# Performance work log

Measured on AMD Instinct MI355X. Metric: run time of the kernel, lower is better.

## Reference

```python
import jax, jax.numpy as jnp
import numpy as np

N = 50000
E = 800000
D_IN = 128
D_EMB = 128
D_OUT = 2
AGGRS = ('sum', 'max', 'mean', 'sum', 'max', 'mean')


def setup_inputs() -> dict:
    key = jax.random.key(0)
    ks = jax.random.split(key, 10)
    x = jax.random.normal(ks[0], (N, D_IN), dtype=jnp.float32)
    edge_index = jax.random.randint(ks[1], (2, E), 0, N, dtype=jnp.int64)
    # 6 SAGEConv layers, all 128->128: lin_l (weight+bias, applied to aggregated
    # neighbors) and lin_r (weight only, applied to root/self features).
    w_l = jax.random.normal(ks[2], (6, D_EMB, D_EMB), dtype=jnp.float32) * 0.05
    b_l = jax.random.normal(ks[3], (6, D_EMB), dtype=jnp.float32) * 0.05
    w_r = jax.random.normal(ks[4], (6, D_EMB, D_EMB), dtype=jnp.float32) * 0.05
    w1 = jax.random.normal(ks[5], (D_EMB, D_EMB), dtype=jnp.float32) * 0.05
    b1 = jax.random.normal(ks[6], (D_EMB,), dtype=jnp.float32) * 0.05
    w2 = jax.random.normal(ks[7], (D_EMB, D_OUT), dtype=jnp.float32) * 0.05
    b2 = jax.random.normal(ks[8], (D_OUT,), dtype=jnp.float32) * 0.05
    return {"x": x, "edge_index": edge_index, "w_l": w_l, "b_l": b_l,
            "w_r": w_r, "w1": w1, "b1": b1, "w2": w2, "b2": b2}


def _aggregate(msg, dst, aggr, num_nodes):
    # msg: [E, D] gathered source features; dst: [E] target node ids.
    if aggr == 'sum':
        return jax.ops.segment_sum(msg, dst, num_segments=num_nodes)
    if aggr == 'max':
        m = jax.ops.segment_max(msg, dst, num_segments=num_nodes)
        # nodes with no incoming edges -> 0 (PyG scatter-max fill)
        return jnp.where(jnp.isfinite(m), m, 0.0)
    # mean
    s = jax.ops.segment_sum(msg, dst, num_segments=num_nodes)
    cnt = jax.ops.segment_sum(jnp.ones((msg.shape[0],), msg.dtype), dst,
                              num_segments=num_nodes)
    return s / jnp.maximum(cnt, 1.0)[:, None]


def _sage_conv(x, src, dst, wl, bl, wr, aggr):
    msg = x[src]                               # [E, D] gather
    agg = _aggregate(msg, dst, aggr, x.shape[0])
    return agg @ wl + bl + x @ wr              # lin_l(aggr) + lin_r(x)


def reference(x, edge_index, w_l, b_l, w_r, w1, b1, w2, b2):
    src, dst = edge_index[0], edge_index[1]    # messages flow src -> dst
    h = x
    for i, aggr in enumerate(AGGRS):
        h = _sage_conv(h, src, dst, w_l[i], b_l[i], w_r[i], aggr)
        h = jax.nn.relu(h)                     # dropout p=0.1 is identity in eval
    h = jax.nn.relu(h @ w1 + b1)
    return h @ w2 + b2
```

## Files before the change

kernel.cpp:

```cpp
#include <hip/hip_runtime.h>

#define NN 50000
#define NE 800000
#define D 128

typedef unsigned short ushort_t;
typedef __attribute__((ext_vector_type(8))) short short8;
typedef __attribute__((ext_vector_type(4))) float f32x4;
typedef __attribute__((ext_vector_type(8))) _Float16 half8;
typedef __attribute__((ext_vector_type(2))) _Float16 half2v;


__global__ void k_hist(const int* __restrict__ dst, int* __restrict__ cnt, int e) {
  int i = blockIdx.x * blockDim.x + threadIdx.x;
  if (i < e) atomicAdd(&cnt[dst[i]], 1);
}

__global__ __launch_bounds__(1024) void k_scan(const int* __restrict__ cnt,
                                               int* __restrict__ row_start,
                                               int* __restrict__ cursor, int n) {
  __shared__ int wsum[16];
  __shared__ int carry_s;
  int t = threadIdx.x;
  int lane = t & 63, wid = t >> 6;
  if (t == 0) carry_s = 0;
  __syncthreads();
  for (int base = 0; base < n; base += 4096) {
    int i = base + t * 4;
    int4 v = make_int4(0, 0, 0, 0);
    if (i + 3 < n) v = *(const int4*)&cnt[i];
    else if (i < n) {
      v.x = cnt[i];
      if (i + 1 < n) v.y = cnt[i + 1];
      if (i + 2 < n) v.z = cnt[i + 2];
    }
    int tot = v.x + v.y + v.z + v.w;
    int x = tot;
    #pragma unroll
    for (int off = 1; off < 64; off <<= 1) {
      int y = __shfl_up(x, off, 64);
      if (lane >= off) x += y;
    }
    if (lane == 63) wsum[wid] = x;
    __syncthreads();
    if (wid == 0) {
      int w = (lane < 16) ? wsum[lane] : 0;
      #pragma unroll
      for (int off = 1; off < 16; off <<= 1) {
        int y = __shfl_up(w, off, 64);
        if (lane >= off) w += y;
      }
      if (lane < 16) wsum[lane] = w;
    }
    __syncthreads();
    int off0 = carry_s + (wid ? wsum[wid - 1] : 0) + (x - tot);
    int4 o;
    o.x = off0;
    o.y = off0 + v.x;
    o.z = off0 + v.x + v.y;
    o.w = off0 + v.x + v.y + v.z;
    if (i + 3 < n) {
      *(int4*)&row_start[i] = o;
      *(int4*)&cursor[i] = o;
    } else if (i < n) {
      row_start[i] = o.x; cursor[i] = o.x;
      if (i + 1 < n) { row_start[i + 1] = o.y; cursor[i + 1] = o.y; }
      if (i + 2 < n) { row_start[i + 2] = o.z; cursor[i + 2] = o.z; }
    }
    __syncthreads();
    if (t == 0) carry_s += wsum[15];
    __syncthreads();
  }
  if (t == 0) row_start[n] = carry_s;
}

__global__ __launch_bounds__(256) void k_scatter(const int* __restrict__ src,
                                                 const int* __restrict__ dst,
                                                 int* __restrict__ cursor,
                                                 int* __restrict__ csr_src, int e) {
  int g = blockIdx.x & 7;
  int i = (blockIdx.x >> 3) * 1024 + threadIdx.x * 4;
  if (i >= e) return;
  int4 s4 = *(const int4*)&src[i];
  int4 d4 = *(const int4*)&dst[i];
  if ((unsigned)d4.x / 6250u == (unsigned)g) { int p = atomicAdd(&cursor[d4.x], 1); csr_src[p] = s4.x; }
  if ((unsigned)d4.y / 6250u == (unsigned)g) { int p = atomicAdd(&cursor[d4.y], 1); csr_src[p] = s4.y; }
  if ((unsigned)d4.z / 6250u == (unsigned)g) { int p = atomicAdd(&cursor[d4.z], 1); csr_src[p] = s4.z; }
  if ((unsigned)d4.w / 6250u == (unsigned)g) { int p = atomicAdd(&cursor[d4.w], 1); csr_src[p] = s4.w; }
}


__global__ __launch_bounds__(256) void k_tofp16(const float* __restrict__ in,
                                                _Float16* __restrict__ out, int n8) {
  int i = blockIdx.x * 256 + threadIdx.x;
  if (i >= n8) return;
  float4 a = ((const float4*)in)[i * 2];
  float4 b = ((const float4*)in)[i * 2 + 1];
  half8 o;
  o[0] = (_Float16)a.x; o[1] = (_Float16)a.y; o[2] = (_Float16)a.z; o[3] = (_Float16)a.w;
  o[4] = (_Float16)b.x; o[5] = (_Float16)b.y; o[6] = (_Float16)b.z; o[7] = (_Float16)b.w;
  ((half8*)out)[i] = o;
}


__global__ void k_wsplit(const float* __restrict__ W, ushort_t* __restrict__ hi,
                         ushort_t* __restrict__ lo, int total) {
  int idx = blockIdx.x * 256 + threadIdx.x;
  if (idx >= total) return;
  int mat = idx >> 14, rem = idx & 16383;
  int k = rem >> 7, c = rem & 127;
  float f = W[idx];
  unsigned u = __float_as_uint(f);
  float lf = f - __uint_as_float(u & 0xffff0000u);
  size_t dst = ((size_t)mat << 14) + (size_t)(k >> 5) * 4096 + c * 32 + (k & 31);
  hi[dst] = (ushort_t)(u >> 16);
  lo[dst] = (ushort_t)(__float_as_uint(lf) >> 16);
}


__device__ __forceinline__ float4 op_add(float4 a, float4 v) {
  a.x += v.x; a.y += v.y; a.z += v.z; a.w += v.w; return a;
}
__device__ __forceinline__ float4 op_max(float4 a, float4 v) {
  a.x = fmaxf(a.x, v.x); a.y = fmaxf(a.y, v.y);
  a.z = fmaxf(a.z, v.z); a.w = fmaxf(a.w, v.w); return a;
}
__device__ __forceinline__ void h8_to_f(half8 v, float4& x, float4& y) {
  x.x = (float)v[0]; x.y = (float)v[1]; x.z = (float)v[2]; x.w = (float)v[3];
  y.x = (float)v[4]; y.y = (float)v[5]; y.z = (float)v[6]; y.w = (float)v[7];
}

template <int AGGR>
__global__ __launch_bounds__(256) void k_aggregate(const _Float16* __restrict__ h,
                                                   const int* __restrict__ csr_src,
                                                   const int* __restrict__ row_start,
                                                   _Float16* __restrict__ agg, int n) {
  int lane = threadIdx.x & 63;
  int node = blockIdx.x * 4 + (threadIdx.x >> 6);
  if (node >= n) return;
  int slot = lane >> 4, c = lane & 15;
  const half8* __restrict__ hp = (const half8*)h;
  int s = row_start[node], e = row_start[node + 1];
  float4 init;
  if (AGGR == 1) init = make_float4(-INFINITY, -INFINITY, -INFINITY, -INFINITY);
  else           init = make_float4(0.f, 0.f, 0.f, 0.f);
  float4 a0x = init, a0y = init, a1x = init, a1y = init;
  int j = s + slot;
  for (; j + 4 < e; j += 8) {
    int i0 = csr_src[j], i1 = csr_src[j + 4];
    half8 v0 = hp[(size_t)i0 * 16 + c];
    half8 v1 = hp[(size_t)i1 * 16 + c];
    float4 v0x, v0y, v1x, v1y;
    h8_to_f(v0, v0x, v0y);
    h8_to_f(v1, v1x, v1y);
    if (AGGR == 1) {
      a0x = op_max(a0x, v0x); a0y = op_max(a0y, v0y);
      a1x = op_max(a1x, v1x); a1y = op_max(a1y, v1y);
    } else {
      a0x = op_add(a0x, v0x); a0y = op_add(a0y, v0y);
      a1x = op_add(a1x, v1x); a1y = op_add(a1y, v1y);
    }
  }
  for (; j < e; j += 4) {
    half8 v0 = hp[(size_t)csr_src[j] * 16 + c];
    float4 v0x, v0y;
    h8_to_f(v0, v0x, v0y);
    if (AGGR == 1) { a0x = op_max(a0x, v0x); a0y = op_max(a0y, v0y); }
    else           { a0x = op_add(a0x, v0x); a0y = op_add(a0y, v0y); }
  }
  float4 rx, ry;
  if (AGGR == 1) { rx = op_max(a0x, a1x); ry = op_max(a0y, a1y); }
  else           { rx = op_add(a0x, a1x); ry = op_add(a0y, a1y); }
  #pragma unroll
  for (int off = 16; off <= 32; off <<= 1) {
    float4 ox, oy;
    ox.x = __shfl_xor(rx.x, off, 64); ox.y = __shfl_xor(rx.y, off, 64);
    ox.z = __shfl_xor(rx.z, off, 64); ox.w = __shfl_xor(rx.w, off, 64);
    oy.x = __shfl_xor(ry.x, off, 64); oy.y = __shfl_xor(ry.y, off, 64);
    oy.z = __shfl_xor(ry.z, off, 64); oy.w = __shfl_xor(ry.w, off, 64);
    if (AGGR == 1) { rx = op_max(rx, ox); ry = op_max(ry, oy); }
    else           { rx = op_add(rx, ox); ry = op_add(ry, oy); }
  }
  if (slot == 0) {
    if (AGGR == 1) {
      if (e == s) { rx = make_float4(0.f,0.f,0.f,0.f); ry = rx; }
    } else if (AGGR == 2) {
      float inv = 1.0f / fmaxf((float)(e - s), 1.0f);
      rx.x *= inv; rx.y *= inv; rx.z *= inv; rx.w *= inv;
      ry.x *= inv; ry.y *= inv; ry.z *= inv; ry.w *= inv;
    }
    half8 o;
    o[0] = (_Float16)rx.x; o[1] = (_Float16)rx.y; o[2] = (_Float16)rx.z; o[3] = (_Float16)rx.w;
    o[4] = (_Float16)ry.x; o[5] = (_Float16)ry.y; o[6] = (_Float16)ry.z; o[7] = (_Float16)ry.w;
    ((half8*)agg)[(size_t)node * 16 + c] = o;
  }
}


#define GBM 64

__global__ __launch_bounds__(256) void k_gemm(
    const _Float16* __restrict__ A1, const ushort_t* __restrict__ Wh1, const ushort_t* __restrict__ Wl1,
    const _Float16* __restrict__ A2, const ushort_t* __restrict__ Wh2, const ushort_t* __restrict__ Wl2,
    const float* __restrict__ bias, _Float16* __restrict__ out, int M, int has2) {
  __shared__ ushort_t Ah[GBM * 40];
  __shared__ ushort_t Al[GBM * 40];
  __shared__ ushort_t Bh[128 * 40];
  __shared__ ushort_t Bl[128 * 40];
  int t = threadIdx.x;
  int lane = t & 63, wid = t >> 6;
  int wr = wid >> 1, wc = wid & 1;
  int l15 = lane & 15, kg = lane >> 4;
  int row0 = blockIdx.x * GBM;

  f32x4 acc[2][4] = {};

  int nmat = has2 ? 2 : 1;
  for (int mat = 0; mat < nmat; ++mat) {
    const _Float16* __restrict__ A = mat ? A2 : A1;
    const ushort_t* __restrict__ Wh = mat ? Wh2 : Wh1;
    const ushort_t* __restrict__ Wl = mat ? Wl2 : Wl1;
    for (int kt = 0; kt < 4; ++kt) {
      __syncthreads();
      {
        int r = t >> 2, cq = t & 3;
        int grow = row0 + r;
        half8 v = {};
        if (grow < M) v = *(const half8*)&A[(size_t)grow * D + kt * 32 + cq * 8];
        unsigned hw[8], lw[8];
        #pragma unroll
        for (int eidx = 0; eidx < 8; ++eidx) {
          float f = (float)v[eidx];
          unsigned u = __float_as_uint(f);
          float lf = f - __uint_as_float(u & 0xffff0000u);
          hw[eidx] = u >> 16;
          lw[eidx] = __float_as_uint(lf) >> 16;
        }
        uint4 hv = make_uint4(hw[0] | (hw[1] << 16), hw[2] | (hw[3] << 16),
                              hw[4] | (hw[5] << 16), hw[6] | (hw[7] << 16));
        uint4 lv = make_uint4(lw[0] | (lw[1] << 16), lw[2] | (lw[3] << 16),
                              lw[4] | (lw[5] << 16), lw[6] | (lw[7] << 16));
        *(uint4*)&Ah[r * 40 + cq * 8] = hv;
        *(uint4*)&Al[r * 40 + cq * 8] = lv;
      }
      {
        int c = t >> 1, q = t & 1;
        const ushort_t* sh = Wh + (size_t)kt * 4096 + t * 16;
        const ushort_t* sl = Wl + (size_t)kt * 4096 + t * 16;
        uint4 a0 = *(const uint4*)sh;
        uint4 a1 = *(const uint4*)(sh + 8);
        uint4 b0 = *(const uint4*)sl;
        uint4 b1 = *(const uint4*)(sl + 8);
        *(uint4*)&Bh[c * 40 + q * 16]     = a0;
        *(uint4*)&Bh[c * 40 + q * 16 + 8] = a1;
        *(uint4*)&Bl[c * 40 + q * 16]     = b0;
        *(uint4*)&Bl[c * 40 + q * 16 + 8] = b1;
      }
      __syncthreads();
      short8 ah[2], al[2], bh[4], bl[4];
      #pragma unroll
      for (int m = 0; m < 2; ++m) {
        int row = wr * 32 + m * 16 + l15;
        ah[m] = *(const short8*)&Ah[row * 40 + kg * 8];
        al[m] = *(const short8*)&Al[row * 40 + kg * 8];
      }
      #pragma unroll
      for (int n = 0; n < 4; ++n) {
        int col = wc * 64 + n * 16 + l15;
        bh[n] = *(const short8*)&Bh[col * 40 + kg * 8];
        bl[n] = *(const short8*)&Bl[col * 40 + kg * 8];
      }
      #pragma unroll
      for (int m = 0; m < 2; ++m)
        #pragma unroll
        for (int n = 0; n < 4; ++n) {
          acc[m][n] = __builtin_amdgcn_mfma_f32_16x16x32_bf16(ah[m], bh[n], acc[m][n], 0, 0, 0);
          acc[m][n] = __builtin_amdgcn_mfma_f32_16x16x32_bf16(ah[m], bl[n], acc[m][n], 0, 0, 0);
          acc[m][n] = __builtin_amdgcn_mfma_f32_16x16x32_bf16(al[m], bh[n], acc[m][n], 0, 0, 0);
        }
    }
  }
  int crow = kg * 4;
  #pragma unroll
  for (int n = 0; n < 4; ++n) {
    int col = wc * 64 + n * 16 + l15;
    float b = bias[col];
    #pragma unroll
    for (int m = 0; m < 2; ++m) {
      int rbase = row0 + wr * 32 + m * 16 + crow;
      #pragma unroll
      for (int q = 0; q < 4; ++q) {
        int grow = rbase + q;
        if (grow < M)
          out[(size_t)grow * D + col] = (_Float16)fmaxf(acc[m][n][q] + b, 0.f);
      }
    }
  }
}


__global__ __launch_bounds__(256) void k_head(const _Float16* __restrict__ h,
                                              const float* __restrict__ w2,
                                              const float* __restrict__ b2,
                                              float* __restrict__ out, int n) {
  int lane = threadIdx.x & 63;
  int node = blockIdx.x * 4 + (threadIdx.x >> 6);
  if (node >= n) return;
  half2v v = *(const half2v*)&h[(size_t)node * D + lane * 2];
  float v0 = (float)v[0], v1 = (float)v[1];
  float4 w = *(const float4*)&w2[lane * 4];
  float p0 = v0 * w.x + v1 * w.z;
  float p1 = v0 * w.y + v1 * w.w;
  #pragma unroll
  for (int off = 32; off; off >>= 1) {
    p0 += __shfl_xor(p0, off, 64);
    p1 += __shfl_xor(p1, off, 64);
  }
  if (lane == 0)
    ((float2*)out)[node] = make_float2(p0 + b2[0], p1 + b2[1]);
}


extern "C" void kernel_launch(void* const* d_in, const int* in_sizes, int n_in,
                              void* d_out, int out_size, void* d_ws, size_t ws_size,
                              hipStream_t stream) {
  const float* x   = (const float*)d_in[0];
  const int*   ei  = (const int*)d_in[1];
  const float* w_l = (const float*)d_in[2];
  const float* b_l = (const float*)d_in[3];
  const float* w_r = (const float*)d_in[4];
  const float* w1  = (const float*)d_in[5];
  const float* b1  = (const float*)d_in[6];
  const float* w2  = (const float*)d_in[7];
  const float* b2  = (const float*)d_in[8];
  float* out = (float*)d_out;

  const int* src = ei;
  const int* dst = ei + NE;

  char* ws = (char*)d_ws;
  size_t SZH = (size_t)NN * D * sizeof(_Float16);
  _Float16* bufX = (_Float16*)ws;
  _Float16* bufA = (_Float16*)(ws + SZH);
  _Float16* bufB = (_Float16*)(ws + 2 * SZH);
  int* csr_src   = (int*)(ws + 3 * SZH);
  int* row_start = (int*)(ws + 3 * SZH + (size_t)NE * sizeof(int));
  int* cursor    = row_start + NN + 2;
  int* cnt       = cursor + NN + 2;
  ushort_t* whi  = (ushort_t*)(cnt + NN + 2);
  ushort_t* wlo  = whi + 13 * 16384;

  k_wsplit<<<(6 * 16384 + 255) / 256, 256, 0, stream>>>(w_l, whi, wlo, 6 * 16384);
  k_wsplit<<<(6 * 16384 + 255) / 256, 256, 0, stream>>>(w_r, whi + 6 * 16384, wlo + 6 * 16384, 6 * 16384);
  k_wsplit<<<(16384 + 255) / 256, 256, 0, stream>>>(w1, whi + 12 * 16384, wlo + 12 * 16384, 16384);
  k_tofp16<<<(NN * D / 8 + 255) / 256, 256, 0, stream>>>(x, bufX, NN * D / 8);

  hipMemsetAsync(cnt, 0, NN * sizeof(int), stream);
  k_hist<<<(NE + 255) / 256, 256, 0, stream>>>(dst, cnt, NE);
  k_scan<<<1, 1024, 0, stream>>>(cnt, row_start, cursor, NN);
  k_scatter<<<8 * ((NE + 1023) / 1024), 256, 0, stream>>>(src, dst, cursor, csr_src, NE);

  const int agg_grid  = (NN + 3) / 4;
  const int gemm_grid = (NN + GBM - 1) / GBM;

  const _Float16* h = bufX;
  _Float16* bufs[2] = {bufA, bufB};
  for (int i = 0; i < 6; ++i) {
    _Float16* aggb = bufs[i & 1];
    switch (i % 3) {
      case 0: k_aggregate<0><<<agg_grid, 256, 0, stream>>>(h, csr_src, row_start, aggb, NN); break;
      case 1: k_aggregate<1><<<agg_grid, 256, 0, stream>>>(h, csr_src, row_start, aggb, NN); break;
      case 2: k_aggregate<2><<<agg_grid, 256, 0, stream>>>(h, csr_src, row_start, aggb, NN); break;
    }
    k_gemm<<<gemm_grid, 256, 0, stream>>>(aggb, whi + (size_t)i * 16384, wlo + (size_t)i * 16384,
                                          h,    whi + (size_t)(6 + i) * 16384, wlo + (size_t)(6 + i) * 16384,
                                          b_l + (size_t)i * D, aggb, NN, 1);
    h = aggb;
  }
  k_gemm<<<gemm_grid, 256, 0, stream>>>(h, whi + (size_t)12 * 16384, wlo + (size_t)12 * 16384,
                                        h, nullptr, nullptr, b1, bufA, NN, 0);
  k_head<<<agg_grid, 256, 0, stream>>>(bufA, w2, b2, out, NN);
}
```

Before: 458.5 us.

## Fuse neighbor aggregation into per-layer GEMM kernel via shared-memory staging

```diff
diff --git a/kernel.cpp b/kernel.cpp
--- a/kernel.cpp
+++ b/kernel.cpp
@@ -130,103 +130,108 @@
   y.x = (float)v[4]; y.y = (float)v[5]; y.z = (float)v[6]; y.w = (float)v[7];
 }
 
+
+#define GBM 64
+
 template <int AGGR>
-__global__ __launch_bounds__(256) void k_aggregate(const _Float16* __restrict__ h,
-                                                   const int* __restrict__ csr_src,
-                                                   const int* __restrict__ row_start,
-                                                   _Float16* __restrict__ agg, int n) {
-  int lane = threadIdx.x & 63;
-  int node = blockIdx.x * 4 + (threadIdx.x >> 6);
-  if (node >= n) return;
-  int slot = lane >> 4, c = lane & 15;
-  const half8* __restrict__ hp = (const half8*)h;
-  int s = row_start[node], e = row_start[node + 1];
-  float4 init;
-  if (AGGR == 1) init = make_float4(-INFINITY, -INFINITY, -INFINITY, -INFINITY);
-  else           init = make_float4(0.f, 0.f, 0.f, 0.f);
-  float4 a0x = init, a0y = init, a1x = init, a1y = init;
-  int j = s + slot;
-  for (; j + 4 < e; j += 8) {
-    int i0 = csr_src[j], i1 = csr_src[j + 4];
-    half8 v0 = hp[(size_t)i0 * 16 + c];
-    half8 v1 = hp[(size_t)i1 * 16 + c];
-    float4 v0x, v0y, v1x, v1y;
-    h8_to_f(v0, v0x, v0y);
-    h8_to_f(v1, v1x, v1y);
-    if (AGGR == 1) {
-      a0x = op_max(a0x, v0x); a0y = op_max(a0y, v0y);
-      a1x = op_max(a1x, v1x); a1y = op_max(a1y, v1y);
-    } else {
-      a0x = op_add(a0x, v0x); a0y = op_add(a0y, v0y);
-      a1x = op_add(a1x, v1x); a1y = op_add(a1y, v1y);
-    }
-  }
-  for (; j < e; j += 4) {
-    half8 v0 = hp[(size_t)csr_src[j] * 16 + c];
-    float4 v0x, v0y;
-    h8_to_f(v0, v0x, v0y);
-    if (AGGR == 1) { a0x = op_max(a0x, v0x); a0y = op_max(a0y, v0y); }
-    else           { a0x = op_add(a0x, v0x); a0y = op_add(a0y, v0y); }
-  }
-  float4 rx, ry;
-  if (AGGR == 1) { rx = op_max(a0x, a1x); ry = op_max(a0y, a1y); }
-  else           { rx = op_add(a0x, a1x); ry = op_add(a0y, a1y); }
-  #pragma unroll
-  for (int off = 16; off <= 32; off <<= 1) {
-    float4 ox, oy;
-    ox.x = __shfl_xor(rx.x, off, 64); ox.y = __shfl_xor(rx.y, off, 64);
-    ox.z = __shfl_xor(rx.z, off, 64); ox.w = __shfl_xor(rx.w, off, 64);
-    oy.x = __shfl_xor(ry.x, off, 64); oy.y = __shfl_xor(ry.y, off, 64);
-    oy.z = __shfl_xor(ry.z, off, 64); oy.w = __shfl_xor(ry.w, off, 64);
-    if (AGGR == 1) { rx = op_max(rx, ox); ry = op_max(ry, oy); }
-    else           { rx = op_add(rx, ox); ry = op_add(ry, oy); }
-  }
-  if (slot == 0) {
-    if (AGGR == 1) {
-      if (e == s) { rx = make_float4(0.f,0.f,0.f,0.f); ry = rx; }
-    } else if (AGGR == 2) {
-      float inv = 1.0f / fmaxf((float)(e - s), 1.0f);
-      rx.x *= inv; rx.y *= inv; rx.z *= inv; rx.w *= inv;
-      ry.x *= inv; ry.y *= inv; ry.z *= inv; ry.w *= inv;
-    }
-    half8 o;
-    o[0] = (_Float16)rx.x; o[1] = (_Float16)rx.y; o[2] = (_Float16)rx.z; o[3] = (_Float16)rx.w;
-    o[4] = (_Float16)ry.x; o[5] = (_Float16)ry.y; o[6] = (_Float16)ry.z; o[7] = (_Float16)ry.w;
-    ((half8*)agg)[(size_t)node * 16 + c] = o;
-  }
-}
-
-
-#define GBM 64
-
-__global__ __launch_bounds__(256) void k_gemm(
-    const _Float16* __restrict__ A1, const ushort_t* __restrict__ Wh1, const ushort_t* __restrict__ Wl1,
-    const _Float16* __restrict__ A2, const ushort_t* __restrict__ Wh2, const ushort_t* __restrict__ Wl2,
-    const float* __restrict__ bias, _Float16* __restrict__ out, int M, int has2) {
+__global__ __launch_bounds__(256) void k_layer(
+    const _Float16* __restrict__ h, const int* __restrict__ csr_src,
+    const int* __restrict__ row_start,
+    const ushort_t* __restrict__ Whl, const ushort_t* __restrict__ Wll,
+    const ushort_t* __restrict__ Whr, const ushort_t* __restrict__ Wlr,
+    const float* __restrict__ bias, _Float16* __restrict__ out, int M) {
+  __shared__ _Float16 Afp[GBM * 136];
   __shared__ ushort_t Ah[GBM * 40];
   __shared__ ushort_t Al[GBM * 40];
   __shared__ ushort_t Bh[128 * 40];
   __shared__ ushort_t Bl[128 * 40];
   int t = threadIdx.x;
   int lane = t & 63, wid = t >> 6;
+  int row0 = blockIdx.x * GBM;
+
+  {
+    int slot = lane >> 4, c = lane & 15;
+    const half8* __restrict__ hp = (const half8*)h;
+    for (int nn = wid; nn < GBM; nn += 4) {
+      int node = row0 + nn;
+      if (node < M) {
+        int s = row_start[node], e = row_start[node + 1];
+        float4 init;
+        if (AGGR == 1) init = make_float4(-INFINITY, -INFINITY, -INFINITY, -INFINITY);
+        else           init = make_float4(0.f, 0.f, 0.f, 0.f);
+        float4 a0x = init, a0y = init, a1x = init, a1y = init;
+        int j = s + slot;
+        for (; j + 4 < e; j += 8) {
+          int i0 = csr_src[j], i1 = csr_src[j + 4];
+          half8 v0 = hp[(size_t)i0 * 16 + c];
+          half8 v1 = hp[(size_t)i1 * 16 + c];
+          float4 v0x, v0y, v1x, v1y;
+          h8_to_f(v0, v0x, v0y);
+          h8_to_f(v1, v1x, v1y);
+          if (AGGR == 1) {
+            a0x = op_max(a0x, v0x); a0y = op_max(a0y, v0y);
+            a1x = op_max(a1x, v1x); a1y = op_max(a1y, v1y);
+          } else {
+            a0x = op_add(a0x, v0x); a0y = op_add(a0y, v0y);
+            a1x = op_add(a1x, v1x); a1y = op_add(a1y, v1y);
+          }
+        }
+        for (; j < e; j += 4) {
+          half8 v0 = hp[(size_t)csr_src[j] * 16 + c];
+          float4 v0x, v0y;
+          h8_to_f(v0, v0x, v0y);
+          if (AGGR == 1) { a0x = op_max(a0x, v0x); a0y = op_max(a0y, v0y); }
+          else           { a0x = op_add(a0x, v0x); a0y = op_add(a0y, v0y); }
+        }
+        float4 rx, ry;
+        if (AGGR == 1) { rx = op_max(a0x, a1x); ry = op_max(a0y, a1y); }
+        else           { rx = op_add(a0x, a1x); ry = op_add(a0y, a1y); }
+        #pragma unroll
+        for (int off = 16; off <= 32; off <<= 1) {
+          float4 ox, oy;
+          ox.x = __shfl_xor(rx.x, off, 64); ox.y = __shfl_xor(rx.y, off, 64);
+          ox.z = __shfl_xor(rx.z, off, 64); ox.w = __shfl_xor(rx.w, off, 64);
+          oy.x = __shfl_xor(ry.x, off, 64); oy.y = __shfl_xor(ry.y, off, 64);
+          oy.z = __shfl_xor(ry.z, off, 64); oy.w = __shfl_xor(ry.w, off, 64);
+          if (AGGR == 1) { rx = op_max(rx, ox); ry = op_max(ry, oy); }
+          else           { rx = op_add(rx, ox); ry = op_add(ry, oy); }
+        }
+        if (slot == 0) {
+          if (AGGR == 1) {
+            if (e == s) { rx = make_float4(0.f,0.f,0.f,0.f); ry = rx; }
+          } else if (AGGR == 2) {
+            float inv = 1.0f / fmaxf((float)(e - s), 1.0f);
+            rx.x *= inv; rx.y *= inv; rx.z *= inv; rx.w *= inv;
+            ry.x *= inv; ry.y *= inv; ry.z *= inv; ry.w *= inv;
+          }
+          half8 o;
+          o[0] = (_Float16)rx.x; o[1] = (_Float16)rx.y; o[2] = (_Float16)rx.z; o[3] = (_Float16)rx.w;
+          o[4] = (_Float16)ry.x; o[5] = (_Float16)ry.y; o[6] = (_Float16)ry.z; o[7] = (_Float16)ry.w;
+          *(half8*)&Afp[nn * 136 + c * 8] = o;
+        }
+      }
+    }
+  }
+
   int wr = wid >> 1, wc = wid & 1;
   int l15 = lane & 15, kg = lane >> 4;
-  int row0 = blockIdx.x * GBM;
 
   f32x4 acc[2][4] = {};
 
-  int nmat = has2 ? 2 : 1;
-  for (int mat = 0; mat < nmat; ++mat) {
-    const _Float16* __restrict__ A = mat ? A2 : A1;
-    const ushort_t* __restrict__ Wh = mat ? Wh2 : Wh1;
-    const ushort_t* __restrict__ Wl = mat ? Wl2 : Wl1;
+  for (int mat = 0; mat < 2; ++mat) {
+    const ushort_t* __restrict__ Wh = mat ? Whr : Whl;
+    const ushort_t* __restrict__ Wl = mat ? Wlr : Wll;
     for (int kt = 0; kt < 4; ++kt) {
       __syncthreads();
       {
         int r = t >> 2, cq = t & 3;
-        int grow = row0 + r;
         half8 v = {};
-        if (grow < M) v = *(const half8*)&A[(size_t)grow * D + kt * 32 + cq * 8];
+        if (mat == 0) {
+          v = *(const half8*)&Afp[r * 136 + kt * 32 + cq * 8];
+        } else {
+          int grow = row0 + r;
+          if (grow < M) v = *(const half8*)&h[(size_t)grow * D + kt * 32 + cq * 8];
+        }
         unsigned hw[8], lw[8];
         #pragma unroll
         for (int eidx = 0; eidx < 8; ++eidx) {
@@ -279,6 +284,99 @@
           acc[m][n] = __builtin_amdgcn_mfma_f32_16x16x32_bf16(al[m], bh[n], acc[m][n], 0, 0, 0);
         }
     }
+  }
+  int crow = kg * 4;
+  #pragma unroll
+  for (int n = 0; n < 4; ++n) {
+    int col = wc * 64 + n * 16 + l15;
+    float b = bias[col];
+    #pragma unroll
+    for (int m = 0; m < 2; ++m) {
+      int rbase = row0 + wr * 32 + m * 16 + crow;
+      #pragma unroll
+      for (int q = 0; q < 4; ++q) {
+        int grow = rbase + q;
+        if (grow < M)
+          out[(size_t)grow * D + col] = (_Float16)fmaxf(acc[m][n][q] + b, 0.f);
+      }
+    }
+  }
+}
+
+
+__global__ __launch_bounds__(256) void k_gemm1(
+    const _Float16* __restrict__ A1, const ushort_t* __restrict__ Wh1, const ushort_t* __restrict__ Wl1,
+    const float* __restrict__ bias, _Float16* __restrict__ out, int M) {
+  __shared__ ushort_t Ah[GBM * 40];
+  __shared__ ushort_t Al[GBM * 40];
+  __shared__ ushort_t Bh[128 * 40];
+  __shared__ ushort_t Bl[128 * 40];
+  int t = threadIdx.x;
+  int lane = t & 63, wid = t >> 6;
+  int wr = wid >> 1, wc = wid & 1;
+  int l15 = lane & 15, kg = lane >> 4;
+  int row0 = blockIdx.x * GBM;
+
+  f32x4 acc[2][4] = {};
+
+  for (int kt = 0; kt < 4; ++kt) {
+    __syncthreads();
+    {
+      int r = t >> 2, cq = t & 3;
+      int grow = row0 + r;
+      half8 v = {};
+      if (grow < M) v = *(const half8*)&A1[(size_t)grow * D + kt * 32 + cq * 8];
+      unsigned hw[8], lw[8];
+      #pragma unroll
+      for (int eidx = 0; eidx < 8; ++eidx) {
+        float f = (float)v[eidx];
+        unsigned u = __float_as_uint(f);
+        float lf = f - __uint_as_float(u & 0xffff0000u);
+        hw[eidx] = u >> 16;
+        lw[eidx] = __float_as_uint(lf) >> 16;
+      }
+      uint4 hv = make_uint4(hw[0] | (hw[1] << 16), hw[2] | (hw[3] << 16),
+                            hw[4] | (hw[5] << 16), hw[6] | (hw[7] << 16));
+      uint4 lv = make_uint4(lw[0] | (lw[1] << 16), lw[2] | (lw[3] << 16),
+                            lw[4] | (lw[5] << 16), lw[6] | (lw[7] << 16));
+      *(uint4*)&Ah[r * 40 + cq * 8] = hv;
+      *(uint4*)&Al[r * 40 + cq * 8] = lv;
+    }
+    {
+      int c = t >> 1, q = t & 1;
+      const ushort_t* sh = Wh1 + (size_t)kt * 4096 + t * 16;
+      const ushort_t* sl = Wl1 + (size_t)kt * 4096 + t * 16;
+      uint4 a0 = *(const uint4*)sh;
+      uint4 a1 = *(const uint4*)(sh + 8);
+      uint4 b0 = *(const uint4*)sl;
+      uint4 b1 = *(const uint4*)(sl + 8);
+      *(uint4*)&Bh[c * 40 + q * 16]     = a0;
+      *(uint4*)&Bh[c * 40 + q * 16 + 8] = a1;
+      *(uint4*)&Bl[c * 40 + q * 16]     = b0;
+      *(uint4*)&Bl[c * 40 + q * 16 + 8] = b1;
+    }
+    __syncthreads();
+    short8 ah[2], al[2], bh[4], bl[4];
+    #pragma unroll
+    for (int m = 0; m < 2; ++m) {
+      int row = wr * 32 + m * 16 + l15;
+      ah[m] = *(const short8*)&Ah[row * 40 + kg * 8];
+      al[m] = *(const short8*)&Al[row * 40 + kg * 8];
+    }
+    #pragma unroll
+    for (int n = 0; n < 4; ++n) {
+      int col = wc * 64 + n * 16 + l15;
+      bh[n] = *(const short8*)&Bh[col * 40 + kg * 8];
+      bl[n] = *(const short8*)&Bl[col * 40 + kg * 8];
+    }
+    #pragma unroll
+    for (int m = 0; m < 2; ++m)
+      #pragma unroll
+      for (int n = 0; n < 4; ++n) {
+        acc[m][n] = __builtin_amdgcn_mfma_f32_16x16x32_bf16(ah[m], bh[n], acc[m][n], 0, 0, 0);
+        acc[m][n] = __builtin_amdgcn_mfma_f32_16x16x32_bf16(ah[m], bl[n], acc[m][n], 0, 0, 0);
+        acc[m][n] = __builtin_amdgcn_mfma_f32_16x16x32_bf16(al[m], bh[n], acc[m][n], 0, 0, 0);
+      }
   }
   int crow = kg * 4;
   #pragma unroll
@@ -360,24 +458,25 @@
   k_scan<<<1, 1024, 0, stream>>>(cnt, row_start, cursor, NN);
   k_scatter<<<8 * ((NE + 1023) / 1024), 256, 0, stream>>>(src, dst, cursor, csr_src, NE);
 
-  const int agg_grid  = (NN + 3) / 4;
-  const int gemm_grid = (NN + GBM - 1) / GBM;
+  const int layer_grid = (NN + GBM - 1) / GBM;
 
   const _Float16* h = bufX;
   _Float16* bufs[2] = {bufA, bufB};
   for (int i = 0; i < 6; ++i) {
-    _Float16* aggb = bufs[i & 1];
+    _Float16* ob = bufs[i & 1];
+    const ushort_t* whl = whi + (size_t)i * 16384;
+    const ushort_t* wll = wlo + (size_t)i * 16384;
+    const ushort_t* whr = whi + (size_t)(6 + i) * 16384;
+    const ushort_t* wlr = wlo + (size_t)(6 + i) * 16384;
+    const float* bl = b_l + (size_t)i * D;
     switch (i % 3) {
-      case 0: k_aggregate<0><<<agg_grid, 256, 0, stream>>>(h, csr_src, row_start, aggb, NN); break;
-      case 1: k_aggregate<1><<<agg_grid, 256, 0, stream>>>(h, csr_src, row_start, aggb, NN); break;
-      case 2: k_aggregate<2><<<agg_grid, 256, 0, stream>>>(h, csr_src, row_start, aggb, NN); break;
-    }
-    k_gemm<<<gemm_grid, 256, 0, stream>>>(aggb, whi + (size_t)i * 16384, wlo + (size_t)i * 16384,
-                                          h,    whi + (size_t)(6 + i) * 16384, wlo + (size_t)(6 + i) * 16384,
-                                          b_l + (size_t)i * D, aggb, NN, 1);
-    h = aggb;
-  }
-  k_gemm<<<gemm_grid, 256, 0, stream>>>(h, whi + (size_t)12 * 16384, wlo + (size_t)12 * 16384,
-                                        h, nullptr, nullptr, b1, bufA, NN, 0);
-  k_head<<<agg_grid, 256, 0, stream>>>(bufA, w2, b2, out, NN);
-}
+      case 0: k_layer<0><<<layer_grid, 256, 0, stream>>>(h, csr_src, row_start, whl, wll, whr, wlr, bl, ob, NN); break;
+      case 1: k_layer<1><<<layer_grid, 256, 0, stream>>>(h, csr_src, row_start, whl, wll, whr, wlr, bl, ob, NN); break;
+      case 2: k_layer<2><<<layer_grid, 256, 0, stream>>>(h, csr_src, row_start, whl, wll, whr, wlr, bl, ob, NN); break;
+    }
+    h = ob;
+  }
+  k_gemm1<<<layer_grid, 256, 0, stream>>>(h, whi + (size_t)12 * 16384, wlo + (size_t)12 * 16384,
+                                          b1, bufA, NN);
+  k_head<<<(NN + 3) / 4, 256, 0, stream>>>(bufA, w2, b2, out, NN);
+}
```

Result: slower. 823.3 us (+79.6%).
